# Performance work log

Hardware: AMD Instinct MI355X
Metric: run time of the kernel (lower is better)

## Reference

```python
import jax, jax.numpy as jnp
import numpy as np

N = 100000   # nodes
E = 1600000  # edges
S = 4        # state_dimension
H = 64       # hidden_channels


def _gcn_conv(x, row, col, W, b):
    """PyG GCNConv: h = x @ W; add self-loops; symmetric deg^-1/2 norm; scatter-add; + bias."""
    n = x.shape[0]
    h = x @ W  # [N, out]
    loop = jnp.arange(n, dtype=row.dtype)
    r = jnp.concatenate([row, loop])  # sources (with self-loops)
    c = jnp.concatenate([col, loop])  # targets (with self-loops)
    deg = jax.ops.segment_sum(jnp.ones(r.shape[0], h.dtype), c, num_segments=n)
    dinv = jnp.where(deg > 0, jax.lax.rsqrt(deg), 0.0)
    norm = dinv[r] * dinv[c]                      # [E+N]
    msg = h[r] * norm[:, None]                    # gather + scale, [E+N, out]
    out = jax.ops.segment_sum(msg, c, num_segments=n)  # scatter-add
    return out + b


def setup_inputs() -> dict:
    key = jax.random.key(0)
    k1, k2, k3, k4 = jax.random.split(key, 4)
    x = jax.random.normal(k1, (N, S), dtype=jnp.float32)
    edge_index = jax.random.randint(k2, (2, E), 0, N, dtype=jnp.int32)
    # Glorot-ish init for the two GCNConv linear layers (+ zero bias, PyG default)
    W1 = jax.random.normal(k3, (S, H), dtype=jnp.float32) * (1.0 / np.sqrt(S))
    b1 = jnp.zeros((H,), jnp.float32)
    W2 = jax.random.normal(k4, (H, S), dtype=jnp.float32) * (1.0 / np.sqrt(H))
    b2 = jnp.zeros((S,), jnp.float32)
    return {"x": x, "edge_index": edge_index, "W1": W1, "b1": b1, "W2": W2, "b2": b2}


def reference(x, edge_index, W1, b1, W2, b2):
    row, col = edge_index[0], edge_index[1]
    h = _gcn_conv(x, row, col, W1, b1)
    h = jax.nn.relu(h)
    out = _gcn_conv(h, row, col, W2, b2)
    return out
```

## Files before the change

### kernel.cpp

```cpp
#include <hip/hip_runtime.h>


#define CSHIFT 10
#define CNODES 1024
#define KC_MAX 128
#define CAPC   18432
#define EPB    2048
#define PTH    256
#define CURPAD 16
#define HCAP   9216
#define ANODES 128
#define ACAP   2432

__global__ void k_zero(int* __restrict__ p, int n) {
    int i = blockIdx.x * blockDim.x + threadIdx.x;
    if (i < n) p[i] = 0;
}

__global__ void __launch_bounds__(PTH) k_part(
        const int* __restrict__ row, const int* __restrict__ col,
        int e, int Kc, int* __restrict__ cursor, unsigned* __restrict__ ere) {
    __shared__ int wh[4][KC_MAX];
    int t = threadIdx.x, w = t >> 6;
    for (int k = t; k < 4 * KC_MAX; k += PTH) ((int*)wh)[k] = 0;
    __syncthreads();
    int lo = blockIdx.x * EPB;
    int cbuf[8], rbuf[8];
#pragma unroll
    for (int k = 0; k < 8; ++k) {
        int i = lo + t + k * PTH;
        if (i < e) { cbuf[k] = col[i]; rbuf[k] = row[i]; }
        else { cbuf[k] = -1; rbuf[k] = 0; }
    }
#pragma unroll
    for (int k = 0; k < 8; ++k)
        if (cbuf[k] >= 0) atomicAdd(&wh[w][cbuf[k] >> CSHIFT], 1);
    __syncthreads();
    if (t < KC_MAX) {
        int s = wh[0][t] + wh[1][t] + wh[2][t] + wh[3][t];
        int gb = 0;
        if (t < Kc && s) gb = atomicAdd(&cursor[t * CURPAD], s);
        int run = gb;
#pragma unroll
        for (int w2 = 0; w2 < 4; ++w2) { int c = wh[w2][t]; wh[w2][t] = run; run += c; }
    }
    __syncthreads();
#pragma unroll
    for (int k = 0; k < 8; ++k) {
        int c = cbuf[k];
        if (c < 0) continue;
        int b = c >> CSHIFT;
        int pos = atomicAdd(&wh[w][b], 1);
        if (pos < CAPC)
            ere[(size_t)b * CAPC + pos] =
                ((unsigned)rbuf[k] << CSHIFT) | (unsigned)(c & (CNODES - 1));
    }
}

__global__ void __launch_bounds__(1024) k_sortH(
        const int* __restrict__ cursor, unsigned* __restrict__ ere,
        int* __restrict__ rstart, const float4* __restrict__ x,
        float* __restrict__ dinv, float4* __restrict__ y, int n) {
    __shared__ int hist[CNODES];
    __shared__ int scn[CNODES];
    __shared__ int cur[CNODES];
    __shared__ unsigned sorted[HCAP];
    int bh = blockIdx.x, b = bh >> 1, h = bh & 1;
    int t = threadIdx.x, nlo = b << CSHIFT;
    hist[t] = 0;
    __syncthreads();
    size_t c0 = (size_t)b * CAPC;
    int m = min(cursor[b * CURPAD], CAPC);
    int n4 = m >> 2;
    const uint4* e4 = (const uint4*)(ere + c0);
    uint4 rb[5];
    int gv[5];
#pragma unroll
    for (int k = 0; k < 5; ++k) {
        int g = t + k * 1024;
        gv[k] = (g < n4);
        if (gv[k]) rb[k] = e4[g];
    }
    unsigned tailrec = 0xFFFFFFFFu;
    {
        int ti = (n4 << 2) + t;
        if (ti < m) tailrec = ere[c0 + ti];
    }
#pragma unroll
    for (int k = 0; k < 5; ++k) {
        if (!gv[k]) continue;
        atomicAdd(&hist[rb[k].x & (CNODES - 1)], 1);
        atomicAdd(&hist[rb[k].y & (CNODES - 1)], 1);
        atomicAdd(&hist[rb[k].z & (CNODES - 1)], 1);
        atomicAdd(&hist[rb[k].w & (CNODES - 1)], 1);
    }
    if (tailrec != 0xFFFFFFFFu) atomicAdd(&hist[tailrec & (CNODES - 1)], 1);
    __syncthreads();
    int hv = hist[t];
    scn[t] = hv;
    __syncthreads();
    for (int off = 1; off < CNODES; off <<= 1) {
        int v = (t >= off) ? scn[t - off] : 0;
        __syncthreads();
        scn[t] += v;
        __syncthreads();
    }
    int st = scn[t] - hv;
    int low = scn[CNODES / 2 - 1];
    rstart[(b << CSHIFT) + t] = (int)c0 + st;
    int base = h ? low : 0;
    cur[t] = st - base;
    if ((t >> 9) == h) {
        int node = nlo + t;
        if (node < n) {
            float di = rsqrtf((float)hv + 1.0f);
            dinv[node] = di;
            float4 xv = x[node];
            y[node] = make_float4(xv.x * di, xv.y * di, xv.z * di, xv.w * di);
        }
    }
    __syncthreads();
#pragma unroll
    for (int k = 0; k < 5; ++k) {
        if (!gv[k]) continue;
        unsigned e0 = rb[k].x, e1 = rb[k].y, e2 = rb[k].z, e3 = rb[k].w;
        int l0 = e0 & (CNODES - 1);
        if ((l0 >> 9) == h) { int p = atomicAdd(&cur[l0], 1); if (p < HCAP) sorted[p] = e0 >> CSHIFT; }
        int l1 = e1 & (CNODES - 1);
        if ((l1 >> 9) == h) { int p = atomicAdd(&cur[l1], 1); if (p < HCAP) sorted[p] = e1 >> CSHIFT; }
        int l2 = e2 & (CNODES - 1);
        if ((l2 >> 9) == h) { int p = atomicAdd(&cur[l2], 1); if (p < HCAP) sorted[p] = e2 >> CSHIFT; }
        int l3 = e3 & (CNODES - 1);
        if ((l3 >> 9) == h) { int p = atomicAdd(&cur[l3], 1); if (p < HCAP) sorted[p] = e3 >> CSHIFT; }
    }
    if (tailrec != 0xFFFFFFFFu) {
        int l = tailrec & (CNODES - 1);
        if ((l >> 9) == h) { int p = atomicAdd(&cur[l], 1); if (p < HCAP) sorted[p] = tailrec >> CSHIFT; }
    }
    __syncthreads();
    int cnt = h ? (m - low) : low;
    int wb = min(cnt, HCAP);
    for (int i = t; i < wb; i += 1024) ere[c0 + base + i] = sorted[i];
}

__global__ void __launch_bounds__(512) k_mid(
        const unsigned* __restrict__ ere, const int* __restrict__ rstart,
        const int* __restrict__ cursor, const float* __restrict__ dinv,
        const float4* __restrict__ x, const float4* __restrict__ y,
        const float* __restrict__ W1, const float* __restrict__ b1,
        const float* __restrict__ W2, const float* __restrict__ b2,
        float4* __restrict__ z, float4* __restrict__ out, int n) {
    __shared__ unsigned recs[ACAP];
    __shared__ float4 sums[ANODES];
    int g = blockIdx.x, t = threadIdx.x;
    int nlo = g * ANODES;
    int b = nlo >> CSHIFT;
    int c0i = (int)((size_t)b * CAPC);
    int s0 = rstart[nlo];
    int e0 = ((g & 7) == 7) ? c0i + min(cursor[b * CURPAD], CAPC)
                            : rstart[nlo + ANODES];
    int len = min(e0 - s0, ACAP);
    for (int i = t; i < len; i += 512) recs[i] = ere[s0 + i];
    __syncthreads();
    int tt = t >> 2, q = t & 3;
    int s = rstart[nlo + tt] - s0;
    int epos = (tt == ANODES - 1) ? len : min(rstart[nlo + tt + 1] - s0, len);
    float vx = 0.f, vy = 0.f, vz = 0.f, vw = 0.f;
    int i = s + q;
    while (i + 12 < epos) {
        int r0 = recs[i], r1 = recs[i + 4], r2 = recs[i + 8], r3 = recs[i + 12];
        float4 a0 = y[r0], a1 = y[r1], a2 = y[r2], a3 = y[r3];
        vx += a0.x + a1.x + a2.x + a3.x;
        vy += a0.y + a1.y + a2.y + a3.y;
        vz += a0.z + a1.z + a2.z + a3.z;
        vw += a0.w + a1.w + a2.w + a3.w;
        i += 16;
    }
    for (; i < epos; i += 4) {
        float4 a = y[recs[i]];
        vx += a.x; vy += a.y; vz += a.z; vw += a.w;
    }
    vx += __shfl_xor(vx, 1); vx += __shfl_xor(vx, 2);
    vy += __shfl_xor(vy, 1); vy += __shfl_xor(vy, 2);
    vz += __shfl_xor(vz, 1); vz += __shfl_xor(vz, 2);
    vw += __shfl_xor(vw, 1); vw += __shfl_xor(vw, 2);
    if (q == 0) sums[tt] = make_float4(vx, vy, vz, vw);
    __syncthreads();
    int node = nlo + t;
    if (t < ANODES && node < n) {
        float di = dinv[node], sl = di * di;
        float4 sv = sums[t];
        float4 xv = x[node];
        float a0 = di * sv.x + xv.x * sl;
        float a1 = di * sv.y + xv.y * sl;
        float a2 = di * sv.z + xv.z * sl;
        float a3 = di * sv.w + xv.w * sl;
        float t0 = 0.f, t1 = 0.f, t2 = 0.f, t3 = 0.f;
#pragma unroll 8
        for (int j = 0; j < 64; ++j) {
            float hh = b1[j] + a0 * W1[j] + a1 * W1[64 + j] + a2 * W1[128 + j] + a3 * W1[192 + j];
            hh = fmaxf(hh, 0.f);
            t0 += hh * W2[j * 4 + 0];
            t1 += hh * W2[j * 4 + 1];
            t2 += hh * W2[j * 4 + 2];
            t3 += hh * W2[j * 4 + 3];
        }
        z[node] = make_float4(t0 * di, t1 * di, t2 * di, t3 * di);
        out[node] = make_float4(b2[0] + t0 * sl, b2[1] + t1 * sl,
                                b2[2] + t2 * sl, b2[3] + t3 * sl);
    }
}

__global__ void __launch_bounds__(512) k_acc2(
        const unsigned* __restrict__ ere, const int* __restrict__ rstart,
        const int* __restrict__ cursor, const float* __restrict__ dinv,
        const float4* __restrict__ z, float4* __restrict__ out, int n) {
    __shared__ unsigned recs[ACAP];
    __shared__ float4 sums[ANODES];
    int g = blockIdx.x, t = threadIdx.x;
    int nlo = g * ANODES;
    int b = nlo >> CSHIFT;
    int c0i = (int)((size_t)b * CAPC);
    int s0 = rstart[nlo];
    int e0 = ((g & 7) == 7) ? c0i + min(cursor[b * CURPAD], CAPC)
                            : rstart[nlo + ANODES];
    int len = min(e0 - s0, ACAP);
    for (int i = t; i < len; i += 512) recs[i] = ere[s0 + i];
    __syncthreads();
    int tt = t >> 2, q = t & 3;
    int s = rstart[nlo + tt] - s0;
    int epos = (tt == ANODES - 1) ? len : min(rstart[nlo + tt + 1] - s0, len);
    float vx = 0.f, vy = 0.f, vz = 0.f, vw = 0.f;
    int i = s + q;
    while (i + 12 < epos) {
        int r0 = recs[i], r1 = recs[i + 4], r2 = recs[i + 8], r3 = recs[i + 12];
        float4 a0 = z[r0], a1 = z[r1], a2 = z[r2], a3 = z[r3];
        vx += a0.x + a1.x + a2.x + a3.x;
        vy += a0.y + a1.y + a2.y + a3.y;
        vz += a0.z + a1.z + a2.z + a3.z;
        vw += a0.w + a1.w + a2.w + a3.w;
        i += 16;
    }
    for (; i < epos; i += 4) {
        float4 a = z[recs[i]];
        vx += a.x; vy += a.y; vz += a.z; vw += a.w;
    }
    vx += __shfl_xor(vx, 1); vx += __shfl_xor(vx, 2);
    vy += __shfl_xor(vy, 1); vy += __shfl_xor(vy, 2);
    vz += __shfl_xor(vz, 1); vz += __shfl_xor(vz, 2);
    vw += __shfl_xor(vw, 1); vw += __shfl_xor(vw, 2);
    if (q == 0) sums[tt] = make_float4(vx, vy, vz, vw);
    __syncthreads();
    int node = nlo + t;
    if (t < ANODES && node < n) {
        float di = dinv[node];
        float4 sv = sums[t];
        float4 o = out[node];
        out[node] = make_float4(o.x + di * sv.x, o.y + di * sv.y,
                                o.z + di * sv.z, o.w + di * sv.w);
    }
}

extern "C" void kernel_launch(void* const* d_in, const int* in_sizes, int n_in,
                              void* d_out, int out_size, void* d_ws, size_t ws_size,
                              hipStream_t stream) {
    const float* x  = (const float*)d_in[0];
    const int* edge = (const int*)d_in[1];
    const float* W1 = (const float*)d_in[2];
    const float* b1 = (const float*)d_in[3];
    const float* W2 = (const float*)d_in[4];
    const float* b2 = (const float*)d_in[5];
    float* out = (float*)d_out;

    const int n = in_sizes[0] / 4;
    const int e = in_sizes[1] / 2;
    const int* row = edge;
    const int* col = edge + e;
    const int Kc = (n + CNODES - 1) >> CSHIFT;

    char* ws = (char*)d_ws;
    float* y    = (float*)ws;  ws += (size_t)4 * n * 4;
    float* zmid = (float*)ws;  ws += (size_t)4 * n * 4;
    float* dinv = (float*)ws;  ws += (size_t)n * 4;
    unsigned* ere = (unsigned*)ws;  ws += (size_t)Kc * CAPC * 4;
    int* cursor = (int*)ws;    ws += (size_t)Kc * CURPAD * 4;
    int* rstart = (int*)ws;    ws += (size_t)Kc * CNODES * 4;

    const int B = 256;
    const int gp = (e + EPB - 1) / EPB;
    const int ga = (n + ANODES - 1) / ANODES;
    const int nz = Kc * CURPAD;

    k_zero<<<(nz + B - 1) / B, B, 0, stream>>>(cursor, nz);
    k_part<<<gp, PTH, 0, stream>>>(row, col, e, Kc, cursor, ere);
    k_sortH<<<2 * Kc, 1024, 0, stream>>>(cursor, ere, rstart, (const float4*)x,
                                         dinv, (float4*)y, n);
    k_mid<<<ga, 512, 0, stream>>>(ere, rstart, cursor, dinv, (const float4*)x,
                                  (const float4*)y, W1, b1, W2, b2,
                                  (float4*)zmid, (float4*)out, n);
    k_acc2<<<ga, 512, 0, stream>>>(ere, rstart, cursor, dinv,
                                   (const float4*)zmid, (float4*)out, n);
}
```

Measured before the change: 136.9 us.

## Replace atomic-cursor edge bucketing with per-block fixed stripes and shuffle scan

The partition kernel now writes each block's edges into a fixed-size per-bucket stripe slot and records per-block counts, instead of reserving space through global atomic cursors. This removes the cursor zeroing kernel and the global atomics. The sort kernel walks the padded stripes using those counts, writes to a separate sorted buffer, and swaps its barrier-heavy prefix scan for a wavefront shuffle scan. The cost is scanning a larger padded stripe region, which is mostly empty slots, and silently dropping edges if any block puts more than 128 edges into one bucket.

```diff
diff --git a/kernel.cpp b/kernel.cpp
--- a/kernel.cpp
+++ b/kernel.cpp
@@ -1,30 +1,26 @@
 #include <hip/hip_runtime.h>
 
 
-#define CSHIFT 10
-#define CNODES 1024
-#define KC_MAX 128
-#define CAPC   18432
-#define EPB    2048
-#define PTH    256
-#define CURPAD 16
-#define HCAP   9216
-#define ANODES 128
-#define ACAP   2432
-
-__global__ void k_zero(int* __restrict__ p, int n) {
-    int i = blockIdx.x * blockDim.x + threadIdx.x;
-    if (i < n) p[i] = 0;
-}
+#define CSHIFT  10
+#define CNODES  1024
+#define EPB     4096
+#define PTH     512
+#define PERBLK  128
+#define PBSHIFT 7
+#define CAPC    18432
+#define HCAP    9216
+#define ANODES  128
+#define ACAP    2432
 
 __global__ void __launch_bounds__(PTH) k_part(
         const int* __restrict__ row, const int* __restrict__ col,
-        int e, int Kc, int* __restrict__ cursor, unsigned* __restrict__ ere) {
-    __shared__ int wh[4][KC_MAX];
-    int t = threadIdx.x, w = t >> 6;
-    for (int k = t; k < 4 * KC_MAX; k += PTH) ((int*)wh)[k] = 0;
-    __syncthreads();
-    int lo = blockIdx.x * EPB;
+        int e, int Kc, int NB, int* __restrict__ cnt,
+        unsigned* __restrict__ stripe) {
+    __shared__ int cur[128];
+    int t = threadIdx.x, bx = blockIdx.x;
+    if (t < 128) cur[t] = 0;
+    __syncthreads();
+    int lo = bx * EPB;
     int cbuf[8], rbuf[8];
 #pragma unroll
     for (int k = 0; k < 8; ++k) {
@@ -32,86 +28,79 @@
         if (i < e) { cbuf[k] = col[i]; rbuf[k] = row[i]; }
         else { cbuf[k] = -1; rbuf[k] = 0; }
     }
-#pragma unroll
-    for (int k = 0; k < 8; ++k)
-        if (cbuf[k] >= 0) atomicAdd(&wh[w][cbuf[k] >> CSHIFT], 1);
-    __syncthreads();
-    if (t < KC_MAX) {
-        int s = wh[0][t] + wh[1][t] + wh[2][t] + wh[3][t];
-        int gb = 0;
-        if (t < Kc && s) gb = atomicAdd(&cursor[t * CURPAD], s);
-        int run = gb;
-#pragma unroll
-        for (int w2 = 0; w2 < 4; ++w2) { int c = wh[w2][t]; wh[w2][t] = run; run += c; }
-    }
-    __syncthreads();
+    size_t sbase = (size_t)bx * PERBLK;
+    size_t bstride = (size_t)NB * PERBLK;
 #pragma unroll
     for (int k = 0; k < 8; ++k) {
         int c = cbuf[k];
         if (c < 0) continue;
         int b = c >> CSHIFT;
-        int pos = atomicAdd(&wh[w][b], 1);
-        if (pos < CAPC)
-            ere[(size_t)b * CAPC + pos] =
+        int j = atomicAdd(&cur[b], 1);
+        if (j < PERBLK)
+            stripe[(size_t)b * bstride + sbase + j] =
                 ((unsigned)rbuf[k] << CSHIFT) | (unsigned)(c & (CNODES - 1));
     }
+    __syncthreads();
+    if (t < Kc) cnt[t * NB + bx] = min(cur[t], PERBLK);
 }
 
 __global__ void __launch_bounds__(1024) k_sortH(
-        const int* __restrict__ cursor, unsigned* __restrict__ ere,
-        int* __restrict__ rstart, const float4* __restrict__ x,
-        float* __restrict__ dinv, float4* __restrict__ y, int n) {
+        const int* __restrict__ cnt, const unsigned* __restrict__ stripe,
+        unsigned* __restrict__ sortedg, int* __restrict__ rstart,
+        int* __restrict__ mtot, const float4* __restrict__ x,
+        float* __restrict__ dinv, float4* __restrict__ y, int n, int NB) {
     __shared__ int hist[CNODES];
-    __shared__ int scn[CNODES];
-    __shared__ int cur[CNODES];
+    __shared__ int cur[512];
+    __shared__ int cntl[512];
     __shared__ unsigned sorted[HCAP];
+    __shared__ int wsum[16], wpre[16];
+    __shared__ int lowsh, msh;
     int bh = blockIdx.x, b = bh >> 1, h = bh & 1;
-    int t = threadIdx.x, nlo = b << CSHIFT;
+    int t = threadIdx.x, lane = t & 63, wv = t >> 6;
+    for (int i = t; i < NB; i += 1024) cntl[i] = cnt[b * NB + i];
     hist[t] = 0;
     __syncthreads();
-    size_t c0 = (size_t)b * CAPC;
-    int m = min(cursor[b * CURPAD], CAPC);
-    int n4 = m >> 2;
-    const uint4* e4 = (const uint4*)(ere + c0);
-    uint4 rb[5];
-    int gv[5];
+    size_t s0 = (size_t)b * NB * PERBLK;
+    int nslot4 = (NB * PERBLK) >> 2;
+    const uint4* st4 = (const uint4*)(stripe + s0);
+    for (int g = t; g < nslot4; g += 1024) {
+        int slot = g << 2;
+        int cb = cntl[slot >> PBSHIFT];
+        int j = slot & (PERBLK - 1);
+        if (j >= cb) continue;
+        uint4 w = st4[g];
+        atomicAdd(&hist[w.x & (CNODES - 1)], 1);
+        if (j + 1 < cb) atomicAdd(&hist[w.y & (CNODES - 1)], 1);
+        if (j + 2 < cb) atomicAdd(&hist[w.z & (CNODES - 1)], 1);
+        if (j + 3 < cb) atomicAdd(&hist[w.w & (CNODES - 1)], 1);
+    }
+    __syncthreads();
+    int hv = hist[t];
+    int v = hv;
 #pragma unroll
-    for (int k = 0; k < 5; ++k) {
-        int g = t + k * 1024;
-        gv[k] = (g < n4);
-        if (gv[k]) rb[k] = e4[g];
-    }
-    unsigned tailrec = 0xFFFFFFFFu;
-    {
-        int ti = (n4 << 2) + t;
-        if (ti < m) tailrec = ere[c0 + ti];
-    }
-#pragma unroll
-    for (int k = 0; k < 5; ++k) {
-        if (!gv[k]) continue;
-        atomicAdd(&hist[rb[k].x & (CNODES - 1)], 1);
-        atomicAdd(&hist[rb[k].y & (CNODES - 1)], 1);
-        atomicAdd(&hist[rb[k].z & (CNODES - 1)], 1);
-        atomicAdd(&hist[rb[k].w & (CNODES - 1)], 1);
-    }
-    if (tailrec != 0xFFFFFFFFu) atomicAdd(&hist[tailrec & (CNODES - 1)], 1);
-    __syncthreads();
-    int hv = hist[t];
-    scn[t] = hv;
-    __syncthreads();
-    for (int off = 1; off < CNODES; off <<= 1) {
-        int v = (t >= off) ? scn[t - off] : 0;
-        __syncthreads();
-        scn[t] += v;
-        __syncthreads();
-    }
-    int st = scn[t] - hv;
-    int low = scn[CNODES / 2 - 1];
-    rstart[(b << CSHIFT) + t] = (int)c0 + st;
+    for (int off = 1; off < 64; off <<= 1) {
+        int u = __shfl_up(v, off);
+        if (lane >= off) v += u;
+    }
+    if (lane == 63) wsum[wv] = v;
+    __syncthreads();
+    if (t < 16) {
+        int s = 0;
+        for (int i = 0; i < t; ++i) s += wsum[i];
+        wpre[t] = s;
+    }
+    __syncthreads();
+    int incl = v + wpre[wv];
+    if (t == 511) lowsh = incl;
+    if (t == 1023) msh = incl;
+    __syncthreads();
+    int st = incl - hv;
+    int low = lowsh, m = msh;
     int base = h ? low : 0;
-    cur[t] = st - base;
     if ((t >> 9) == h) {
-        int node = nlo + t;
+        cur[t & 511] = st - base;
+        rstart[(b << CSHIFT) + t] = b * CAPC + st;
+        int node = (b << CSHIFT) + t;
         if (node < n) {
             float di = rsqrtf((float)hv + 1.0f);
             dinv[node] = di;
@@ -119,33 +108,33 @@
             y[node] = make_float4(xv.x * di, xv.y * di, xv.z * di, xv.w * di);
         }
     }
-    __syncthreads();
-#pragma unroll
-    for (int k = 0; k < 5; ++k) {
-        if (!gv[k]) continue;
-        unsigned e0 = rb[k].x, e1 = rb[k].y, e2 = rb[k].z, e3 = rb[k].w;
-        int l0 = e0 & (CNODES - 1);
-        if ((l0 >> 9) == h) { int p = atomicAdd(&cur[l0], 1); if (p < HCAP) sorted[p] = e0 >> CSHIFT; }
-        int l1 = e1 & (CNODES - 1);
-        if ((l1 >> 9) == h) { int p = atomicAdd(&cur[l1], 1); if (p < HCAP) sorted[p] = e1 >> CSHIFT; }
-        int l2 = e2 & (CNODES - 1);
-        if ((l2 >> 9) == h) { int p = atomicAdd(&cur[l2], 1); if (p < HCAP) sorted[p] = e2 >> CSHIFT; }
-        int l3 = e3 & (CNODES - 1);
-        if ((l3 >> 9) == h) { int p = atomicAdd(&cur[l3], 1); if (p < HCAP) sorted[p] = e3 >> CSHIFT; }
-    }
-    if (tailrec != 0xFFFFFFFFu) {
-        int l = tailrec & (CNODES - 1);
-        if ((l >> 9) == h) { int p = atomicAdd(&cur[l], 1); if (p < HCAP) sorted[p] = tailrec >> CSHIFT; }
-    }
-    __syncthreads();
-    int cnt = h ? (m - low) : low;
-    int wb = min(cnt, HCAP);
-    for (int i = t; i < wb; i += 1024) ere[c0 + base + i] = sorted[i];
+    if (t == 0 && h == 0) mtot[b] = m;
+    __syncthreads();
+    for (int g = t; g < nslot4; g += 1024) {
+        int slot = g << 2;
+        int cb = cntl[slot >> PBSHIFT];
+        int j = slot & (PERBLK - 1);
+        if (j >= cb) continue;
+        uint4 w = st4[g];
+        int l0 = w.x & (CNODES - 1);
+        if ((l0 >> 9) == h) { int p = atomicAdd(&cur[l0 & 511], 1); if (p < HCAP) sorted[p] = w.x >> CSHIFT; }
+        if (j + 1 < cb) { int l = w.y & (CNODES - 1);
+            if ((l >> 9) == h) { int p = atomicAdd(&cur[l & 511], 1); if (p < HCAP) sorted[p] = w.y >> CSHIFT; } }
+        if (j + 2 < cb) { int l = w.z & (CNODES - 1);
+            if ((l >> 9) == h) { int p = atomicAdd(&cur[l & 511], 1); if (p < HCAP) sorted[p] = w.z >> CSHIFT; } }
+        if (j + 3 < cb) { int l = w.w & (CNODES - 1);
+            if ((l >> 9) == h) { int p = atomicAdd(&cur[l & 511], 1); if (p < HCAP) sorted[p] = w.w >> CSHIFT; } }
+    }
+    __syncthreads();
+    int cown = h ? (m - low) : low;
+    int wb = min(cown, HCAP);
+    size_t d0 = (size_t)b * CAPC + base;
+    for (int i = t; i < wb; i += 1024) sortedg[d0 + i] = sorted[i];
 }
 
 __global__ void __launch_bounds__(512) k_mid(
         const unsigned* __restrict__ ere, const int* __restrict__ rstart,
-        const int* __restrict__ cursor, const float* __restrict__ dinv,
+        const int* __restrict__ mtot, const float* __restrict__ dinv,
         const float4* __restrict__ x, const float4* __restrict__ y,
         const float* __restrict__ W1, const float* __restrict__ b1,
         const float* __restrict__ W2, const float* __restrict__ b2,
@@ -155,9 +144,8 @@
     int g = blockIdx.x, t = threadIdx.x;
     int nlo = g * ANODES;
     int b = nlo >> CSHIFT;
-    int c0i = (int)((size_t)b * CAPC);
     int s0 = rstart[nlo];
-    int e0 = ((g & 7) == 7) ? c0i + min(cursor[b * CURPAD], CAPC)
+    int e0 = ((g & 7) == 7) ? b * CAPC + min(mtot[b], CAPC)
                             : rstart[nlo + ANODES];
     int len = min(e0 - s0, ACAP);
     for (int i = t; i < len; i += 512) recs[i] = ere[s0 + i];
@@ -213,16 +201,15 @@
 
 __global__ void __launch_bounds__(512) k_acc2(
         const unsigned* __restrict__ ere, const int* __restrict__ rstart,
-        const int* __restrict__ cursor, const float* __restrict__ dinv,
+        const int* __restrict__ mtot, const float* __restrict__ dinv,
         const float4* __restrict__ z, float4* __restrict__ out, int n) {
     __shared__ unsigned recs[ACAP];
     __shared__ float4 sums[ANODES];
     int g = blockIdx.x, t = threadIdx.x;
     int nlo = g * ANODES;
     int b = nlo >> CSHIFT;
-    int c0i = (int)((size_t)b * CAPC);
     int s0 = rstart[nlo];
-    int e0 = ((g & 7) == 7) ? c0i + min(cursor[b * CURPAD], CAPC)
+    int e0 = ((g & 7) == 7) ? b * CAPC + min(mtot[b], CAPC)
                             : rstart[nlo + ANODES];
     int len = min(e0 - s0, ACAP);
     for (int i = t; i < len; i += 512) recs[i] = ere[s0 + i];
@@ -277,27 +264,27 @@
     const int* row = edge;
     const int* col = edge + e;
     const int Kc = (n + CNODES - 1) >> CSHIFT;
+    const int NB = (e + EPB - 1) / EPB;
 
     char* ws = (char*)d_ws;
     float* y    = (float*)ws;  ws += (size_t)4 * n * 4;
     float* zmid = (float*)ws;  ws += (size_t)4 * n * 4;
     float* dinv = (float*)ws;  ws += (size_t)n * 4;
-    unsigned* ere = (unsigned*)ws;  ws += (size_t)Kc * CAPC * 4;
-    int* cursor = (int*)ws;    ws += (size_t)Kc * CURPAD * 4;
+    unsigned* stripe = (unsigned*)ws;  ws += (size_t)Kc * NB * PERBLK * 4;
+    unsigned* sortedg = (unsigned*)ws; ws += (size_t)Kc * CAPC * 4;
+    int* cnt    = (int*)ws;    ws += (size_t)Kc * NB * 4;
     int* rstart = (int*)ws;    ws += (size_t)Kc * CNODES * 4;
-
-    const int B = 256;
-    const int gp = (e + EPB - 1) / EPB;
+    int* mtot   = (int*)ws;    ws += (size_t)Kc * 4;
+
     const int ga = (n + ANODES - 1) / ANODES;
-    const int nz = Kc * CURPAD;
-
-    k_zero<<<(nz + B - 1) / B, B, 0, stream>>>(cursor, nz);
-    k_part<<<gp, PTH, 0, stream>>>(row, col, e, Kc, cursor, ere);
-    k_sortH<<<2 * Kc, 1024, 0, stream>>>(cursor, ere, rstart, (const float4*)x,
-                                         dinv, (float4*)y, n);
-    k_mid<<<ga, 512, 0, stream>>>(ere, rstart, cursor, dinv, (const float4*)x,
+
+    k_part<<<NB, PTH, 0, stream>>>(row, col, e, Kc, NB, cnt, stripe);
+    k_sortH<<<2 * Kc, 1024, 0, stream>>>(cnt, stripe, sortedg, rstart, mtot,
+                                         (const float4*)x, dinv, (float4*)y,
+                                         n, NB);
+    k_mid<<<ga, 512, 0, stream>>>(sortedg, rstart, mtot, dinv, (const float4*)x,
                                   (const float4*)y, W1, b1, W2, b2,
                                   (float4*)zmid, (float4*)out, n);
-    k_acc2<<<ga, 512, 0, stream>>>(ere, rstart, cursor, dinv,
+    k_acc2<<<ga, 512, 0, stream>>>(sortedg, rstart, mtot, dinv,
                                    (const float4*)zmid, (float4*)out, n);
 }
```

New measurement: 125.7 us. -8.1%, faster.
